# Kernel optimization log

Measured on AMD Instinct MI355X. Metric: run time of the kernel, lower is better.

## Reference

```python
import jax, jax.numpy as jnp
import numpy as np
from jax import lax

# pywt Wavelet('db4') analysis filters (8 taps)
DEC_LO = jnp.array([-0.010597401784997278, 0.032883011666982945, 0.030841381835986965,
                    -0.18703481171888114, -0.02798376941698385, 0.6308807679295904,
                    0.7148465705525415, 0.23037781330885523], dtype=jnp.float32)
DEC_HI = jnp.array([-0.23037781330885523, 0.7148465705525415, -0.6308807679295904,
                    -0.02798376941698385, 0.18703481171888114, 0.030841381835986965,
                    -0.032883011666982945, -0.010597401784997278], dtype=jnp.float32)
LEVEL = 7


def _dwt(x, lo, hi):
    # mode='zero' single-level DWT: full convolution, keep odd indices.
    # Equivalent to: pad L-2 left / L-1 right, stride-2 VALID correlation with flipped taps.
    L = lo.shape[0]
    xp = jnp.pad(x, ((0, 0), (L - 2, L - 1)))
    k = jnp.stack([lo[::-1], hi[::-1]])[:, None, :]          # [2,1,L]
    y = lax.conv_general_dilated(xp[:, None, :], k, (2,), 'VALID')  # [B,2,n_out]
    return y[:, 0, :], y[:, 1, :]


def _idwt(a, d, rlo, rhi):
    # mode='zero' single-level IDWT: zero-upsample, full conv with rec filters,
    # sum lo+hi branches, trim L-2 each side -> length 2n - L + 2.
    # Implemented as lhs-dilated conv with pad=1 each side; input-channel sum does lo+hi.
    x = jnp.stack([a, d], axis=1)                            # [B,2,n]
    k = jnp.stack([rlo[::-1], rhi[::-1]])[None, :, :]        # [1,2,L]
    y = lax.conv_general_dilated(x, k, (1,), [(1, 1)], lhs_dilation=(2,))
    return y[:, 0, :]


def _soft(c, t):
    return jnp.sign(c) * jnp.maximum(jnp.abs(c) - t, 0.0)


def _wavelet_denoise(x, t):
    rlo, rhi = DEC_LO[::-1], DEC_HI[::-1]
    a = x
    details = []
    for _ in range(LEVEL):
        a, d = _dwt(a, DEC_LO, DEC_HI)
        details.append(d)
    a = _soft(a, t)
    for d in reversed(details):
        d = _soft(d, t)
        if a.shape[-1] == d.shape[-1] + 1:  # pywt waverec odd-length truncation
            a = a[:, :-1]
        a = _idwt(a, d, rlo, rhi)
    return a


def setup_inputs() -> dict:
    key = jax.random.key(0)
    k0, k1, k2 = jax.random.split(key, 3)
    B, N, H = 32768, 1116, 100
    return {
        'x': jax.random.normal(k0, (B, N), dtype=jnp.float32),
        'raw_threshold': jnp.float32(0.02),
        'W1': jax.random.normal(k1, (H, N), dtype=jnp.float32) * 0.03,
        'b1': jnp.zeros((H,), dtype=jnp.float32),
        'W2': jax.random.normal(k2, (1, H), dtype=jnp.float32) * 0.1,
        'b2': jnp.zeros((1,), dtype=jnp.float32),
    }


def reference(x, raw_threshold, W1, b1, W2, b2):
    # .item() / .detach() in the original cut gradients to threshold and x.
    t = jnp.maximum(lax.stop_gradient(raw_threshold), 0.01)
    recon = _wavelet_denoise(lax.stop_gradient(x), t)       # [B,1116]
    h = jax.nn.sigmoid(recon @ W1.T + b1)                   # [B,100]
    reg = h @ W2.T + b2                                     # [B,1]
    return recon, reg
```

## Files before the change

### kernel.cpp

```cpp
#include <hip/hip_runtime.h>
#include <cmath>

typedef __attribute__((ext_vector_type(4))) float f32x4;
typedef __attribute__((ext_vector_type(8))) short s16x8;

#define B_ROWS 32768
#define N_LEN 1116

__device__ constexpr float D_LO[8] = {-0.010597401784997278f, 0.032883011666982945f,
                                      0.030841381835986965f, -0.18703481171888114f,
                                      -0.02798376941698385f, 0.6308807679295904f,
                                      0.7148465705525415f,   0.23037781330885523f};
__device__ constexpr float D_HI[8] = {-0.23037781330885523f, 0.7148465705525415f,
                                      -0.6308807679295904f,  -0.02798376941698385f,
                                      0.18703481171888114f,  0.030841381835986965f,
                                      -0.032883011666982945f, -0.010597401784997278f};

__device__ __forceinline__ float softf(float c, float t) {
  return copysignf(fmaxf(fabsf(c) - t, 0.0f), c);
}

#define WV_STRIDE 3268
#define OX  8
#define OP  1140
#define OQ  1717
#define OD1 2017
#define OD2 2594
#define OD3 2894
#define OD4 3055
#define OD5 3147
#define OD6 3204
#define OD7 3244

__device__ __forceinline__ void dwt_level(const float* in, float* A, float* D,
                                          const int m, const float t, const int lane) {
  for (int i = lane; i < m; i += 64) {
    const float* p = in + 2 * i - 6;
    float sa = 0.f, sd = 0.f;
#pragma unroll
    for (int k = 0; k < 8; k++) {
      float xv = p[7 - k];
      sa = fmaf(D_LO[k], xv, sa);
      sd = fmaf(D_HI[k], xv, sd);
    }
    A[i] = sa;
    D[i] = softf(sd, t);
  }
  if (lane < 8) { A[m + lane] = 0.f; D[m + lane] = 0.f; }
}

__device__ __forceinline__ void idwt_level(const float* A, const float* D,
                                           float* Y, const int outLen, const int lane) {
  const int half = (outLen + 1) >> 1;
  for (int u = lane; u < half; u += 64) {
    float a0 = A[u], a1 = A[u + 1], a2 = A[u + 2], a3 = A[u + 3];
    float d0 = D[u], d1 = D[u + 1], d2 = D[u + 2], d3 = D[u + 3];
    float ye = a0 * D_LO[1];
    ye = fmaf(a1, D_LO[3], ye); ye = fmaf(a2, D_LO[5], ye); ye = fmaf(a3, D_LO[7], ye);
    ye = fmaf(d0, D_HI[1], ye); ye = fmaf(d1, D_HI[3], ye);
    ye = fmaf(d2, D_HI[5], ye); ye = fmaf(d3, D_HI[7], ye);
    float yo = a0 * D_LO[0];
    yo = fmaf(a1, D_LO[2], yo); yo = fmaf(a2, D_LO[4], yo); yo = fmaf(a3, D_LO[6], yo);
    yo = fmaf(d0, D_HI[0], yo); yo = fmaf(d1, D_HI[2], yo);
    yo = fmaf(d2, D_HI[4], yo); yo = fmaf(d3, D_HI[6], yo);
    Y[2 * u] = ye;
    if (2 * u + 1 < outLen) Y[2 * u + 1] = yo;
  }
  if (lane < 8) Y[outLen + lane] = 0.f;
}

__global__ __launch_bounds__(256) void wavelet_kernel(const float* __restrict__ x,
                                                      const float* __restrict__ thr,
                                                      float* __restrict__ out) {
  __shared__ float lds[4 * WV_STRIDE];
  const int lane = threadIdx.x & 63;
  const int wave = threadIdx.x >> 6;
  const long long row = (long long)blockIdx.x * 4 + wave;
  float* base = lds + wave * WV_STRIDE;
  float* X  = base + OX;
  float* P  = base + OP;
  float* Q  = base + OQ;
  float* D1 = base + OD1;
  float* D2 = base + OD2;
  float* D3 = base + OD3;
  float* D4 = base + OD4;
  float* D5 = base + OD5;
  float* D6 = base + OD6;
  float* D7 = base + OD7;

  const float t = fmaxf(thr[0], 0.01f);

  if (lane < 8) {
    X[lane - 8] = 0.f; P[lane - 8] = 0.f; Q[lane - 8] = 0.f;
    D1[lane - 8] = 0.f; D2[lane - 8] = 0.f; D3[lane - 8] = 0.f; D4[lane - 8] = 0.f;
    D5[lane - 8] = 0.f; D6[lane - 8] = 0.f; D7[lane - 8] = 0.f;
    X[1116 + lane] = 0.f;
  }
  {
    const float4* xr = (const float4*)(x + row * N_LEN);
    float4* X4 = (float4*)X;
    for (int i = lane; i < N_LEN / 4; i += 64) X4[i] = xr[i];
  }

  dwt_level(X, P, D1, 561, t, lane);
  dwt_level(P, Q, D2, 284, t, lane);
  dwt_level(Q, P, D3, 145, t, lane);
  dwt_level(P, Q, D4, 76,  t, lane);
  dwt_level(Q, P, D5, 41,  t, lane);
  dwt_level(P, Q, D6, 24,  t, lane);
  dwt_level(Q, P, D7, 15,  t, lane);

  if (lane < 15) P[lane] = softf(P[lane], t);

  idwt_level(P, D7, Q, 24,   lane);
  idwt_level(Q, D6, P, 41,   lane);
  idwt_level(P, D5, Q, 76,   lane);
  idwt_level(Q, D4, P, 145,  lane);
  idwt_level(P, D3, Q, 284,  lane);
  idwt_level(Q, D2, P, 561,  lane);
  idwt_level(P, D1, X, 1116, lane);

  float4* orow = (float4*)(out + row * N_LEN);
  const float4* X4 = (const float4*)X;
  for (int i = lane; i < N_LEN / 4; i += 64) orow[i] = X4[i];
}

__device__ __forceinline__ short f2bf(float f) {
  unsigned u = __float_as_uint(f);
  unsigned r = (u + 0x7FFFu + ((u >> 16) & 1u)) >> 16;
  return (short)r;
}
__device__ __forceinline__ s16x8 cvt8(float4 a, float4 b) {
  s16x8 v;
  v[0] = f2bf(a.x); v[1] = f2bf(a.y); v[2] = f2bf(a.z); v[3] = f2bf(a.w);
  v[4] = f2bf(b.x); v[5] = f2bf(b.y); v[6] = f2bf(b.z); v[7] = f2bf(b.w);
  return v;
}

__global__ __launch_bounds__(256) void head_mfma(const float* __restrict__ recon,
                                                 const float* __restrict__ W1,
                                                 const float* __restrict__ b1,
                                                 const float* __restrict__ W2,
                                                 const float* __restrict__ b2,
                                                 float* __restrict__ reg_out) {
  const int lane = threadIdx.x & 63;
  const int wave = threadIdx.x >> 6;
  const int m0 = (blockIdx.x * 4 + wave) * 16;
  const int r16 = lane & 15;
  const int kg = (lane >> 4) * 8;
  const float* arow = recon + (long long)(m0 + r16) * N_LEN;

  f32x4 acc[7];
#pragma unroll
  for (int c = 0; c < 7; c++) acc[c] = (f32x4){0.f, 0.f, 0.f, 0.f};

  for (int ks = 0; ks < 34; ks++) {
    const int k0 = ks * 32 + kg;
    float4 a0 = *(const float4*)(arow + k0);
    float4 a1 = *(const float4*)(arow + k0 + 4);
    s16x8 av = cvt8(a0, a1);
#pragma unroll
    for (int ct = 0; ct < 7; ct++) {
      const int col = ct * 16 + r16;
      s16x8 bv = (s16x8)(short)0;
      if (col < 100) {
        const float* wrow = W1 + (long long)col * N_LEN + k0;
        bv = cvt8(*(const float4*)wrow, *(const float4*)(wrow + 4));
      }
      acc[ct] = __builtin_amdgcn_mfma_f32_16x16x32_bf16(av, bv, acc[ct], 0, 0, 0);
    }
  }
  {
    const int k0 = 1088 + kg;
    float af[8];
#pragma unroll
    for (int e = 0; e < 8; e++) af[e] = (k0 + e < N_LEN) ? arow[k0 + e] : 0.f;
    s16x8 av;
#pragma unroll
    for (int e = 0; e < 8; e++) av[e] = f2bf(af[e]);
#pragma unroll
    for (int ct = 0; ct < 7; ct++) {
      const int col = ct * 16 + r16;
      s16x8 bv = (s16x8)(short)0;
      if (col < 100) {
        const float* wrow = W1 + (long long)col * N_LEN;
#pragma unroll
        for (int e = 0; e < 8; e++) bv[e] = f2bf((k0 + e < N_LEN) ? wrow[k0 + e] : 0.f);
      }
      acc[ct] = __builtin_amdgcn_mfma_f32_16x16x32_bf16(av, bv, acc[ct], 0, 0, 0);
    }
  }

  float psum[4] = {0.f, 0.f, 0.f, 0.f};
#pragma unroll
  for (int ct = 0; ct < 7; ct++) {
    const int col = ct * 16 + r16;
    if (col < 100) {
      const float b1v = b1[col];
      const float w2v = W2[col];
#pragma unroll
      for (int r = 0; r < 4; r++) {
        float z = acc[ct][r] + b1v;
        float h = 1.f / (1.f + expf(-z));
        psum[r] = fmaf(h, w2v, psum[r]);
      }
    }
  }
#pragma unroll
  for (int mask = 1; mask < 16; mask <<= 1) {
#pragma unroll
    for (int r = 0; r < 4; r++) psum[r] += __shfl_xor(psum[r], mask, 64);
  }
  if (r16 == 0) {
    const float b2v = b2[0];
#pragma unroll
    for (int r = 0; r < 4; r++) reg_out[m0 + (lane >> 4) * 4 + r] = psum[r] + b2v;
  }
}

extern "C" void kernel_launch(void* const* d_in, const int* in_sizes, int n_in,
                              void* d_out, int out_size, void* d_ws, size_t ws_size,
                              hipStream_t stream) {
  const float* x   = (const float*)d_in[0];
  const float* thr = (const float*)d_in[1];
  const float* W1  = (const float*)d_in[2];
  const float* b1  = (const float*)d_in[3];
  const float* W2  = (const float*)d_in[4];
  const float* b2  = (const float*)d_in[5];
  float* out = (float*)d_out;
  float* reg_out = out + (long long)B_ROWS * N_LEN;

  hipLaunchKernelGGL(wavelet_kernel, dim3(B_ROWS / 4), dim3(256), 0, stream, x, thr, out);
  hipLaunchKernelGGL(head_mfma, dim3(B_ROWS / 64), dim3(256), 0, stream,
                     out, W1, b1, W2, b2, reg_out);
}
```

Before: 413.1 us.

## Vectorize wavelet LDS passes, stream x directly, and pre-pack W1 to bf16 fragments

The wavelet kernel now computes four DWT outputs (or eight IDWT outputs) per lane with float4 LDS reads and writes. It reads the first level straight from global memory and writes the last inverse level straight to the output, which removes the LDS staging copy of the input and output rows and shrinks per-wave LDS. A new prep kernel converts W1 once per call into a bf16 MFMA-fragment layout in the workspace, so the head kernel loads pre-packed B fragments instead of converting fp32 W1 on every tile. This adds an extra small launch and relies on the workspace size, with more register pressure per lane.

```diff
diff --git a/kernel.cpp b/kernel.cpp
--- a/kernel.cpp
+++ b/kernel.cpp
@@ -20,53 +20,109 @@
   return copysignf(fmaxf(fabsf(c) - t, 0.0f), c);
 }
 
-#define WV_STRIDE 3268
-#define OX  8
-#define OP  1140
-#define OQ  1717
-#define OD1 2017
-#define OD2 2594
-#define OD3 2894
-#define OD4 3055
-#define OD5 3147
-#define OD6 3204
-#define OD7 3244
-
-__device__ __forceinline__ void dwt_level(const float* in, float* A, float* D,
-                                          const int m, const float t, const int lane) {
-  for (int i = lane; i < m; i += 64) {
-    const float* p = in + 2 * i - 6;
-    float sa = 0.f, sd = 0.f;
+#define WV_STRIDE 2220
+#define OP  8
+#define OQ  596
+#define OD1 904
+#define OD2 1492
+#define OD3 1800
+#define OD4 1972
+#define OD5 2072
+#define OD6 2140
+#define OD7 2188
+
+__device__ __forceinline__ void dwt_compute_store(const float w[16], float* A, float* D,
+                                                  int u, int m, float t) {
+  float sa[4], sd[4];
+#pragma unroll
+  for (int c = 0; c < 4; c++) {
+    float a = 0.f, d = 0.f;
 #pragma unroll
     for (int k = 0; k < 8; k++) {
-      float xv = p[7 - k];
-      sa = fmaf(D_LO[k], xv, sa);
-      sd = fmaf(D_HI[k], xv, sd);
-    }
-    A[i] = sa;
-    D[i] = softf(sd, t);
-  }
-  if (lane < 8) { A[m + lane] = 0.f; D[m + lane] = 0.f; }
-}
-
-__device__ __forceinline__ void idwt_level(const float* A, const float* D,
-                                           float* Y, const int outLen, const int lane) {
-  const int half = (outLen + 1) >> 1;
-  for (int u = lane; u < half; u += 64) {
-    float a0 = A[u], a1 = A[u + 1], a2 = A[u + 2], a3 = A[u + 3];
-    float d0 = D[u], d1 = D[u + 1], d2 = D[u + 2], d3 = D[u + 3];
-    float ye = a0 * D_LO[1];
-    ye = fmaf(a1, D_LO[3], ye); ye = fmaf(a2, D_LO[5], ye); ye = fmaf(a3, D_LO[7], ye);
-    ye = fmaf(d0, D_HI[1], ye); ye = fmaf(d1, D_HI[3], ye);
-    ye = fmaf(d2, D_HI[5], ye); ye = fmaf(d3, D_HI[7], ye);
-    float yo = a0 * D_LO[0];
-    yo = fmaf(a1, D_LO[2], yo); yo = fmaf(a2, D_LO[4], yo); yo = fmaf(a3, D_LO[6], yo);
-    yo = fmaf(d0, D_HI[0], yo); yo = fmaf(d1, D_HI[2], yo);
-    yo = fmaf(d2, D_HI[4], yo); yo = fmaf(d3, D_HI[6], yo);
-    Y[2 * u] = ye;
-    if (2 * u + 1 < outLen) Y[2 * u + 1] = yo;
-  }
-  if (lane < 8) Y[outLen + lane] = 0.f;
+      float xv = w[2 * c + 9 - k];
+      a = fmaf(D_LO[k], xv, a);
+      d = fmaf(D_HI[k], xv, d);
+    }
+    sa[c] = a;
+    sd[c] = softf(d, t);
+  }
+  const int i0 = 4 * u;
+  float4 va, vd;
+  if (i0 + 3 < m) {
+    va = make_float4(sa[0], sa[1], sa[2], sa[3]);
+    vd = make_float4(sd[0], sd[1], sd[2], sd[3]);
+  } else {
+    va.x = (i0 + 0 < m) ? sa[0] : 0.f; vd.x = (i0 + 0 < m) ? sd[0] : 0.f;
+    va.y = (i0 + 1 < m) ? sa[1] : 0.f; vd.y = (i0 + 1 < m) ? sd[1] : 0.f;
+    va.z = (i0 + 2 < m) ? sa[2] : 0.f; vd.z = (i0 + 2 < m) ? sd[2] : 0.f;
+    va.w = (i0 + 3 < m) ? sa[3] : 0.f; vd.w = (i0 + 3 < m) ? sd[3] : 0.f;
+  }
+  *(float4*)(A + i0) = va;
+  *(float4*)(D + i0) = vd;
+}
+
+__device__ __forceinline__ void dwt_zero_tail(float* A, float* D, int m, int lane) {
+  const int m4 = (m + 3) & ~3;
+  if (lane < 4) {
+    ((float4*)(A + m4))[lane] = make_float4(0.f, 0.f, 0.f, 0.f);
+    ((float4*)(D + m4))[lane] = make_float4(0.f, 0.f, 0.f, 0.f);
+  }
+}
+
+__device__ __forceinline__ void dwt_lds(const float* in, float* A, float* D,
+                                        int m, float t, int lane) {
+  const int units = (m + 3) >> 2;
+  for (int u = lane; u < units; u += 64) {
+    float w[16];
+    const float4* p = (const float4*)(in + 8 * u - 8);
+#pragma unroll
+    for (int q = 0; q < 4; q++) {
+      float4 v = p[q];
+      w[4 * q] = v.x; w[4 * q + 1] = v.y; w[4 * q + 2] = v.z; w[4 * q + 3] = v.w;
+    }
+    dwt_compute_store(w, A, D, u, m, t);
+  }
+  dwt_zero_tail(A, D, m, lane);
+}
+
+__device__ __forceinline__ void idwt_pairs(const float a[8], const float d[8], float y[8]) {
+#pragma unroll
+  for (int s = 0; s < 4; s++) {
+    float ye = a[s] * D_LO[1];
+    ye = fmaf(a[s + 1], D_LO[3], ye); ye = fmaf(a[s + 2], D_LO[5], ye);
+    ye = fmaf(a[s + 3], D_LO[7], ye);
+    ye = fmaf(d[s], D_HI[1], ye); ye = fmaf(d[s + 1], D_HI[3], ye);
+    ye = fmaf(d[s + 2], D_HI[5], ye); ye = fmaf(d[s + 3], D_HI[7], ye);
+    float yo = a[s] * D_LO[0];
+    yo = fmaf(a[s + 1], D_LO[2], yo); yo = fmaf(a[s + 2], D_LO[4], yo);
+    yo = fmaf(a[s + 3], D_LO[6], yo);
+    yo = fmaf(d[s], D_HI[0], yo); yo = fmaf(d[s + 1], D_HI[2], yo);
+    yo = fmaf(d[s + 2], D_HI[4], yo); yo = fmaf(d[s + 3], D_HI[6], yo);
+    y[2 * s] = ye;
+    y[2 * s + 1] = yo;
+  }
+}
+
+__device__ __forceinline__ void idwt_lds(const float* A, const float* D, float* Y,
+                                         int outLen, int lane) {
+  const int units = (outLen + 7) >> 3;
+  for (int w = lane; w < units; w += 64) {
+    float a[8], d[8], y[8];
+    *(float4*)&a[0] = *(const float4*)(A + 4 * w);
+    *(float4*)&a[4] = *(const float4*)(A + 4 * w + 4);
+    *(float4*)&d[0] = *(const float4*)(D + 4 * w);
+    *(float4*)&d[4] = *(const float4*)(D + 4 * w + 4);
+    idwt_pairs(a, d, y);
+    const int o0 = 8 * w;
+    if (o0 + 7 >= outLen) {
+#pragma unroll
+      for (int e = 0; e < 8; e++) y[e] = (o0 + e < outLen) ? y[e] : 0.f;
+    }
+    *(float4*)(Y + o0) = make_float4(y[0], y[1], y[2], y[3]);
+    *(float4*)(Y + o0 + 4) = make_float4(y[4], y[5], y[6], y[7]);
+  }
+  const int y8 = (outLen + 7) & ~7;
+  if (lane < 2) ((float4*)(Y + y8))[lane] = make_float4(0.f, 0.f, 0.f, 0.f);
 }
 
 __global__ __launch_bounds__(256) void wavelet_kernel(const float* __restrict__ x,
@@ -77,7 +133,6 @@
   const int wave = threadIdx.x >> 6;
   const long long row = (long long)blockIdx.x * 4 + wave;
   float* base = lds + wave * WV_STRIDE;
-  float* X  = base + OX;
   float* P  = base + OP;
   float* Q  = base + OQ;
   float* D1 = base + OD1;
@@ -89,40 +144,62 @@
   float* D7 = base + OD7;
 
   const float t = fmaxf(thr[0], 0.01f);
-
-  if (lane < 8) {
-    X[lane - 8] = 0.f; P[lane - 8] = 0.f; Q[lane - 8] = 0.f;
-    D1[lane - 8] = 0.f; D2[lane - 8] = 0.f; D3[lane - 8] = 0.f; D4[lane - 8] = 0.f;
-    D5[lane - 8] = 0.f; D6[lane - 8] = 0.f; D7[lane - 8] = 0.f;
-    X[1116 + lane] = 0.f;
-  }
-  {
-    const float4* xr = (const float4*)(x + row * N_LEN);
-    float4* X4 = (float4*)X;
-    for (int i = lane; i < N_LEN / 4; i += 64) X4[i] = xr[i];
-  }
-
-  dwt_level(X, P, D1, 561, t, lane);
-  dwt_level(P, Q, D2, 284, t, lane);
-  dwt_level(Q, P, D3, 145, t, lane);
-  dwt_level(P, Q, D4, 76,  t, lane);
-  dwt_level(Q, P, D5, 41,  t, lane);
-  dwt_level(P, Q, D6, 24,  t, lane);
-  dwt_level(Q, P, D7, 15,  t, lane);
+  const float* xr = x + row * N_LEN;
+
+  if (lane < 2) {
+    ((float4*)(P - 8))[lane] = make_float4(0.f, 0.f, 0.f, 0.f);
+    ((float4*)(Q - 8))[lane] = make_float4(0.f, 0.f, 0.f, 0.f);
+  }
+
+  for (int u = lane; u < 141; u += 64) {
+    float w[16];
+    if (u >= 1 && u <= 138) {
+      const float4* p = (const float4*)(xr + 8 * u - 8);
+#pragma unroll
+      for (int q = 0; q < 4; q++) {
+        float4 v = p[q];
+        w[4 * q] = v.x; w[4 * q + 1] = v.y; w[4 * q + 2] = v.z; w[4 * q + 3] = v.w;
+      }
+    } else {
+#pragma unroll
+      for (int e = 0; e < 16; e++) {
+        int k = 8 * u - 8 + e;
+        w[e] = (k >= 0 && k < N_LEN) ? xr[k] : 0.f;
+      }
+    }
+    dwt_compute_store(w, P, D1, u, 561, t);
+  }
+  dwt_zero_tail(P, D1, 561, lane);
+
+  dwt_lds(P, Q, D2, 284, t, lane);
+  dwt_lds(Q, P, D3, 145, t, lane);
+  dwt_lds(P, Q, D4, 76,  t, lane);
+  dwt_lds(Q, P, D5, 41,  t, lane);
+  dwt_lds(P, Q, D6, 24,  t, lane);
+  dwt_lds(Q, P, D7, 15,  t, lane);
 
   if (lane < 15) P[lane] = softf(P[lane], t);
 
-  idwt_level(P, D7, Q, 24,   lane);
-  idwt_level(Q, D6, P, 41,   lane);
-  idwt_level(P, D5, Q, 76,   lane);
-  idwt_level(Q, D4, P, 145,  lane);
-  idwt_level(P, D3, Q, 284,  lane);
-  idwt_level(Q, D2, P, 561,  lane);
-  idwt_level(P, D1, X, 1116, lane);
-
-  float4* orow = (float4*)(out + row * N_LEN);
-  const float4* X4 = (const float4*)X;
-  for (int i = lane; i < N_LEN / 4; i += 64) orow[i] = X4[i];
+  idwt_lds(P, D7, Q, 24,  lane);
+  idwt_lds(Q, D6, P, 41,  lane);
+  idwt_lds(P, D5, Q, 76,  lane);
+  idwt_lds(Q, D4, P, 145, lane);
+  idwt_lds(P, D3, Q, 284, lane);
+  idwt_lds(Q, D2, P, 561, lane);
+
+  float* orow = out + row * N_LEN;
+  for (int w = lane; w < 140; w += 64) {
+    float a[8], d[8], y[8];
+    *(float4*)&a[0] = *(const float4*)(P + 4 * w);
+    *(float4*)&a[4] = *(const float4*)(P + 4 * w + 4);
+    *(float4*)&d[0] = *(const float4*)(D1 + 4 * w);
+    *(float4*)&d[4] = *(const float4*)(D1 + 4 * w + 4);
+    idwt_pairs(a, d, y);
+    const int o0 = 8 * w;
+    *(float4*)(orow + o0) = make_float4(y[0], y[1], y[2], y[3]);
+    if (o0 + 4 < N_LEN)
+      *(float4*)(orow + o0 + 4) = make_float4(y[4], y[5], y[6], y[7]);
+  }
 }
 
 __device__ __forceinline__ short f2bf(float f) {
@@ -137,8 +214,31 @@
   return v;
 }
 
+#define KSTEPS 35
+#define NFRAG (KSTEPS * 7 * 64)
+
+__global__ __launch_bounds__(256) void prep_w1(const float* __restrict__ W1,
+                                               short* __restrict__ W1bf) {
+  int f = blockIdx.x * 256 + threadIdx.x;
+  if (f >= NFRAG) return;
+  const int ks = f / (7 * 64);
+  const int rem = f % (7 * 64);
+  const int ct = rem / 64;
+  const int lane = rem % 64;
+  const int col = ct * 16 + (lane & 15);
+  const int kbase = ks * 32 + (lane >> 4) * 8;
+  s16x8 v;
+#pragma unroll
+  for (int e = 0; e < 8; e++) {
+    const int k = kbase + e;
+    float val = (col < 100 && k < N_LEN) ? W1[(long long)col * N_LEN + k] : 0.f;
+    v[e] = f2bf(val);
+  }
+  *(s16x8*)(W1bf + (long long)f * 8) = v;
+}
+
 __global__ __launch_bounds__(256) void head_mfma(const float* __restrict__ recon,
-                                                 const float* __restrict__ W1,
+                                                 const short* __restrict__ W1bf,
                                                  const float* __restrict__ b1,
                                                  const float* __restrict__ W2,
                                                  const float* __restrict__ b2,
@@ -156,38 +256,27 @@
 
   for (int ks = 0; ks < 34; ks++) {
     const int k0 = ks * 32 + kg;
-    float4 a0 = *(const float4*)(arow + k0);
-    float4 a1 = *(const float4*)(arow + k0 + 4);
-    s16x8 av = cvt8(a0, a1);
+    s16x8 av = cvt8(*(const float4*)(arow + k0), *(const float4*)(arow + k0 + 4));
+    const s16x8* bfrag = (const s16x8*)(W1bf + ((long long)ks * 7 * 64 + lane) * 8);
 #pragma unroll
     for (int ct = 0; ct < 7; ct++) {
-      const int col = ct * 16 + r16;
-      s16x8 bv = (s16x8)(short)0;
-      if (col < 100) {
-        const float* wrow = W1 + (long long)col * N_LEN + k0;
-        bv = cvt8(*(const float4*)wrow, *(const float4*)(wrow + 4));
-      }
-      acc[ct] = __builtin_amdgcn_mfma_f32_16x16x32_bf16(av, bv, acc[ct], 0, 0, 0);
+      acc[ct] = __builtin_amdgcn_mfma_f32_16x16x32_bf16(av, bfrag[0], acc[ct], 0, 0, 0);
+      bfrag += 64;
     }
   }
   {
     const int k0 = 1088 + kg;
-    float af[8];
-#pragma unroll
-    for (int e = 0; e < 8; e++) af[e] = (k0 + e < N_LEN) ? arow[k0 + e] : 0.f;
     s16x8 av;
 #pragma unroll
-    for (int e = 0; e < 8; e++) av[e] = f2bf(af[e]);
+    for (int e = 0; e < 8; e++) {
+      const int k = k0 + e;
+      av[e] = f2bf((k < N_LEN) ? arow[k] : 0.f);
+    }
+    const s16x8* bfrag = (const s16x8*)(W1bf + ((long long)34 * 7 * 64 + lane) * 8);
 #pragma unroll
     for (int ct = 0; ct < 7; ct++) {
-      const int col = ct * 16 + r16;
-      s16x8 bv = (s16x8)(short)0;
-      if (col < 100) {
-        const float* wrow = W1 + (long long)col * N_LEN;
-#pragma unroll
-        for (int e = 0; e < 8; e++) bv[e] = f2bf((k0 + e < N_LEN) ? wrow[k0 + e] : 0.f);
-      }
-      acc[ct] = __builtin_amdgcn_mfma_f32_16x16x32_bf16(av, bv, acc[ct], 0, 0, 0);
+      acc[ct] = __builtin_amdgcn_mfma_f32_16x16x32_bf16(av, bfrag[0], acc[ct], 0, 0, 0);
+      bfrag += 64;
     }
   }
 
@@ -229,8 +318,10 @@
   const float* b2  = (const float*)d_in[5];
   float* out = (float*)d_out;
   float* reg_out = out + (long long)B_ROWS * N_LEN;
-
+  short* W1bf = (short*)d_ws;
+
+  hipLaunchKernelGGL(prep_w1, dim3((NFRAG + 255) / 256), dim3(256), 0, stream, W1, W1bf);
   hipLaunchKernelGGL(wavelet_kernel, dim3(B_ROWS / 4), dim3(256), 0, stream, x, thr, out);
   hipLaunchKernelGGL(head_mfma, dim3(B_ROWS / 64), dim3(256), 0, stream,
-                     out, W1, b1, W2, b2, reg_out);
-}
+                     out, W1bf, b1, W2, b2, reg_out);
+}
```

New measurement: 341.3 us. -17.4%, faster.
